# Kernel tuning notes

Hardware: AMD Instinct MI355X
Metric: run time of the kernel (lower is better)

The kernel has to match this reference:

```python
import jax, jax.numpy as jnp
import numpy as np

N, E, F_IN, H, C, G, NCLS, L = 50000, 600000, 128, 4, 64, 64, 3, 3
HC = H * C  # 256


def gatv2_layer(x, src, dst, Wl, bl, Wr, br, att, bias):
    # PyG GATv2Conv (concat=True, negative_slope=0.2, share_weights=False),
    # eval mode so attention dropout is identity.
    n = x.shape[0]
    xl = (x @ Wl + bl).reshape(n, H, C)  # source transform
    xr = (x @ Wr + br).reshape(n, H, C)  # target transform
    e = jax.nn.leaky_relu(xl[src] + xr[dst], negative_slope=0.2)  # [E',H,C]
    score = jnp.einsum('ehc,hc->eh', e, att)                      # [E',H]
    # softmax over incoming edges of each destination node
    mx = jax.ops.segment_max(score, dst, num_segments=n)
    ex = jnp.exp(score - mx[dst])
    denom = jax.ops.segment_sum(ex, dst, num_segments=n)
    alpha = ex / denom[dst]                                       # [E',H]
    out = jax.ops.segment_sum(alpha[..., None] * xl[src], dst, num_segments=n)
    return out.reshape(n, HC) + bias


def setup_inputs() -> dict:
    key = jax.random.key(0)
    ks = jax.random.split(key, 32)
    d = {}
    d['x'] = jax.random.normal(ks[0], (N, F_IN), dtype=jnp.float32)
    d['edge_index'] = jax.random.randint(ks[1], (2, E), 0, N, dtype=jnp.int64)
    d['batch'] = jnp.sort(jax.random.randint(ks[2], (N,), 0, G, dtype=jnp.int64))
    k = 3
    for li in range(L):
        fin = F_IN if li == 0 else HC
        s = 1.0 / np.sqrt(fin)
        d[f'Wl{li}'] = jax.random.normal(ks[k], (fin, HC), dtype=jnp.float32) * s; k += 1
        d[f'bl{li}'] = jnp.zeros((HC,), dtype=jnp.float32)
        d[f'Wr{li}'] = jax.random.normal(ks[k], (fin, HC), dtype=jnp.float32) * s; k += 1
        d[f'br{li}'] = jnp.zeros((HC,), dtype=jnp.float32)
        d[f'att{li}'] = jax.random.normal(ks[k], (H, C), dtype=jnp.float32) * (1.0 / np.sqrt(C)); k += 1
        d[f'bias{li}'] = jnp.zeros((HC,), dtype=jnp.float32)
    d['Wout'] = jax.random.normal(ks[k], (HC, NCLS), dtype=jnp.float32) * (1.0 / np.sqrt(HC))
    d['bout'] = jnp.zeros((NCLS,), dtype=jnp.float32)
    return d


def reference(x, edge_index, batch,
              Wl0, bl0, Wr0, br0, att0, bias0,
              Wl1, bl1, Wr1, br1, att1, bias1,
              Wl2, bl2, Wr2, br2, att2, bias2,
              Wout, bout):
    # add self loops (add_self_loops=True)
    loops = jnp.arange(N, dtype=edge_index.dtype)
    src = jnp.concatenate([edge_index[0], loops])
    dst = jnp.concatenate([edge_index[1], loops])

    h = gatv2_layer(x, src, dst, Wl0, bl0, Wr0, br0, att0, bias0)
    for (Wl, bl, Wr, br, att, bias) in [(Wl1, bl1, Wr1, br1, att1, bias1),
                                        (Wl2, bl2, Wr2, br2, att2, bias2)]:
        h = jax.nn.relu(h)
        h = gatv2_layer(h, src, dst, Wl, bl, Wr, br, att, bias)

    # pooling=0: mean + max over graphs
    counts = jax.ops.segment_sum(jnp.ones((N,), dtype=h.dtype), batch, num_segments=G)
    mean_p = jax.ops.segment_sum(h, batch, num_segments=G) / jnp.maximum(counts, 1.0)[:, None]
    max_p = jax.ops.segment_max(h, batch, num_segments=G)
    p = mean_p + max_p
    # dropout is identity in eval mode
    logits = p @ Wout + bout
    return jax.nn.softmax(logits, axis=1)
```

## Files before the change

### kernel.cpp

```cpp
#include <hip/hip_runtime.h>
#include <math.h>

#define N_NODES 50000
#define N_EDGES 600000
#define F_INPUT 128
#define HCDIM 256
#define NGRAPH 64
#define NCLS 3
#define MPAD 50048
#define SCAN_NB ((N_NODES + 255) / 256)
#define LOG2E 1.4426950408889634f
#define NPART 32
#define COLX_PAD 16
#define TOTAL_E (N_EDGES + N_NODES)
#define PLANE64 ((size_t)N_NODES * 64)
#define EDGE_CHUNKS ((N_NODES + 63) / 64)
#define DBINS 64
#define BSEG (SCAN_NB / 4)
#define GEMM_NB ((MPAD / 128) * 4)

#define HIST_NB   ((N_EDGES + N_NODES + 255) / 256)
#define BND_NB    ((N_NODES + 255) / 256)
#define SPLITX_NB (MPAD * F_INPUT / 4 / 256)
#define ZERO_NB   (((MPAD - N_NODES) * HCDIM / 4 + 255) / 256)
#define WPREP_NB  (512 * (F_INPUT + HCDIM + HCDIM) / 256)
#define HP_NB     (HIST_NB + BND_NB + SPLITX_NB + ZERO_NB + WPREP_NB)
#define FILL_NB   ((TOTAL_E + COLX_PAD + 255) / 256)
#define FG_NB     (FILL_NB + GEMM_NB)

typedef float f32x4 __attribute__((ext_vector_type(4)));
typedef float f32x2 __attribute__((ext_vector_type(2)));
typedef _Float16 f16x8 __attribute__((ext_vector_type(8)));
typedef _Float16 f16x4 __attribute__((ext_vector_type(4)));
typedef _Float16 h2 __attribute__((ext_vector_type(2)));

__device__ __forceinline__ void gl_lds16(const void* g, void* l) {
    __builtin_amdgcn_global_load_lds(
        (const __attribute__((address_space(1))) unsigned int*)g,
        (__attribute__((address_space(3))) unsigned int*)l, 16, 0, 0);
}

__device__ __forceinline__ h2 bch2(unsigned int u) { return __builtin_bit_cast(h2, u); }
__device__ __forceinline__ h2 pk16(float a, float b) {
    return __builtin_bit_cast(h2, __builtin_amdgcn_cvt_pkrtz(a, b));
}

__device__ __forceinline__ int xcd_swizzle(int bid, int nwg) {
    int c = bid & 7, idx = bid >> 3;
    int q = nwg >> 3, r = nwg & 7;
    return (c < r) ? c * (q + 1) + idx : r * (q + 1) + (c - r) * q + idx;
}

__device__ __forceinline__ float quad_reduce_add(float p) {
    int s1 = __builtin_amdgcn_update_dpp(0, __builtin_bit_cast(int, p), 0xB1, 0xF, 0xF, true);
    p += __builtin_bit_cast(float, s1);
    int s2 = __builtin_amdgcn_update_dpp(0, __builtin_bit_cast(int, p), 0x4E, 0xF, 0xF, true);
    p += __builtin_bit_cast(float, s2);
    return p;
}

__device__ __forceinline__ void gemm_body_128(
    const _Float16* __restrict__ A, const _Float16* __restrict__ B, int K,
    const float* __restrict__ bl, const float* __restrict__ br,
    unsigned char* __restrict__ xl8, _Float16* __restrict__ xrh,
    _Float16* sA, _Float16* sB, int bx, int by)
{
    int tid = threadIdx.x;
    int lane = tid & 63, wave = tid >> 6;
    int wm = wave >> 1, wn = wave & 1;
    int row0 = bx * 128;
    int n0 = by * 128;
    int quad = lane >> 4, l16 = lane & 15;

    f32x4 acc[4][4];
    #pragma unroll
    for (int i = 0; i < 4; ++i)
        #pragma unroll
        for (int j = 0; j < 4; ++j)
            acc[i][j] = (f32x4){0.f, 0.f, 0.f, 0.f};

    for (int k0 = 0; k0 < K; k0 += 64) {
        __syncthreads();
        #pragma unroll
        for (int pass = 0; pass < 4; ++pass) {
            int c = tid + pass * 256;
            int r = c >> 3;
            int pl = c & 7;
            int pg = pl ^ (r & 7);
            size_t ga = (size_t)(row0 + r) * K + k0 + pg * 8;
            gl_lds16(A + ga, sA + c * 8);
        }
        #pragma unroll
        for (int pass = 0; pass < 4; ++pass) {
            int c = tid + pass * 256;
            int r = c >> 3;
            int pl = c & 7;
            int pg = pl ^ (r & 7);
            size_t gb = (size_t)(n0 + r) * K + k0 + pg * 8;
            gl_lds16(B + gb, sB + c * 8);
        }
        __syncthreads();

        #pragma unroll
        for (int kk = 0; kk < 2; ++kk) {
            f16x8 fa[4], fb[4];
            #pragma unroll
            for (int i = 0; i < 4; ++i) {
                int rr = wm * 64 + i * 16 + l16;
                int ca = (kk * 4 + quad) ^ (rr & 7);
                fa[i] = *(const f16x8*)&sA[rr * 64 + ca * 8];
            }
            #pragma unroll
            for (int j = 0; j < 4; ++j) {
                int nn = wn * 64 + j * 16 + l16;
                int cb = (kk * 4 + quad) ^ (nn & 7);
                fb[j] = *(const f16x8*)&sB[nn * 64 + cb * 8];
            }
            #pragma unroll
            for (int i = 0; i < 4; ++i)
                #pragma unroll
                for (int j = 0; j < 4; ++j)
                    acc[i][j] = __builtin_amdgcn_mfma_f32_16x16x32_f16(fa[i], fb[j], acc[i][j], 0, 0, 0);
        }
    }

    if (by < 2) {
        int cb0 = by * 128;
        #pragma unroll
        for (int j = 0; j < 4; ++j) {
            int col = cb0 + wn * 64 + j * 16 + l16;
            float bj = bl[col];
            int hh = col >> 6, c64 = col & 63;
            unsigned char* xlp = xl8 + (size_t)hh * PLANE64;
            #pragma unroll
            for (int i = 0; i < 4; ++i) {
                int rbase = row0 + wm * 64 + i * 16 + quad * 4;
                #pragma unroll
                for (int r = 0; r < 4; ++r) {
                    int row = rbase + r;
                    if (row < N_NODES) {
                        float v = acc[i][j][r] + bj;
                        int pk = __builtin_amdgcn_cvt_pk_fp8_f32(v, v, 0, false);
                        xlp[(size_t)row * 64 + c64] = (unsigned char)pk;
                    }
                }
            }
        }
    } else {
        int cb0 = (by - 2) * 128;
        #pragma unroll
        for (int j = 0; j < 4; ++j) {
            int col = cb0 + wn * 64 + j * 16 + l16;
            float bj = br[col];
            int hh = col >> 6, c64 = col & 63;
            _Float16* xrp = xrh + (size_t)hh * PLANE64;
            #pragma unroll
            for (int i = 0; i < 4; ++i) {
                int rbase = row0 + wm * 64 + i * 16 + quad * 4;
                #pragma unroll
                for (int r = 0; r < 4; ++r) {
                    int row = rbase + r;
                    if (row < N_NODES)
                        xrp[(size_t)row * 64 + c64] = (_Float16)(acc[i][j][r] + bj);
                }
            }
        }
    }
}

__global__ void hist_prep_kernel(
    const int* __restrict__ ei, int* __restrict__ deg,
    const int* __restrict__ batch, int* __restrict__ startg, int* __restrict__ endg,
    const float* __restrict__ x, _Float16* __restrict__ A,
    _Float16* __restrict__ Bt0, _Float16* __restrict__ Bt1, _Float16* __restrict__ Bt2,
    const float* __restrict__ Wl0, const float* __restrict__ Wr0,
    const float* __restrict__ Wl1, const float* __restrict__ Wr1,
    const float* __restrict__ Wl2, const float* __restrict__ Wr2)
{
    int b = blockIdx.x;
    if (b < HIST_NB) {
        int i = b * 256 + threadIdx.x;
        if (i >= TOTAL_E) return;
        int d = (i < N_EDGES) ? ei[N_EDGES + i] : (i - N_EDGES);
        atomicAdd(&deg[d], 1);
        return;
    }
    b -= HIST_NB;
    if (b < BND_NB) {
        int i = b * 256 + threadIdx.x;
        if (i >= N_NODES) return;
        int g = batch[i];
        if (i == 0 || batch[i - 1] != g) startg[g] = i;
        if (i == N_NODES - 1 || batch[i + 1] != g) endg[g] = i + 1;
        return;
    }
    b -= BND_NB;
    if (b < SPLITX_NB) {
        int base = (b * 256 + threadIdx.x) * 4;
        int row = base >> 7;
        float4 v = make_float4(0.f, 0.f, 0.f, 0.f);
        if (row < N_NODES) v = *(const float4*)&x[base];
        f16x4 o;
        o.x = (_Float16)v.x; o.y = (_Float16)v.y; o.z = (_Float16)v.z; o.w = (_Float16)v.w;
        *(f16x4*)&A[base] = o;
    } else if (b < SPLITX_NB + ZERO_NB) {
        int i = ((b - SPLITX_NB) * 256 + threadIdx.x) * 4;
        if (i < (MPAD - N_NODES) * HCDIM) {
            f16x4 z = {(_Float16)0.f, (_Float16)0.f, (_Float16)0.f, (_Float16)0.f};
            *(f16x4*)&A[(size_t)N_NODES * HCDIM + i] = z;
        }
    } else {
        int t = (b - SPLITX_NB - ZERO_NB) * 256 + threadIdx.x;
        const float* Wl; const float* Wr; _Float16* Bt; int K;
        if (t < 512 * F_INPUT)            { Wl = Wl0; Wr = Wr0; Bt = Bt0; K = F_INPUT; }
        else if (t < 512 * (F_INPUT + HCDIM)) { t -= 512 * F_INPUT; Wl = Wl1; Wr = Wr1; Bt = Bt1; K = HCDIM; }
        else                              { t -= 512 * (F_INPUT + HCDIM); Wl = Wl2; Wr = Wr2; Bt = Bt2; K = HCDIM; }
        int n = t & 511, k = t >> 9;
        float w = (n < 256) ? Wl[k * 256 + n] : Wr[k * 256 + (n - 256)];
        Bt[n * K + k] = (_Float16)w;
    }
}

__global__ void block_scan_kernel(const int* __restrict__ deg, int* __restrict__ rowptr,
                                  int* __restrict__ bsums) {
    __shared__ int wt[4];
    int b = blockIdx.x, t = threadIdx.x, lane = t & 63, wid = t >> 6;
    int i = b * 256 + t;
    int v = (i < N_NODES) ? deg[i] : 0;
    int x = v;
    #pragma unroll
    for (int off = 1; off < 64; off <<= 1) {
        int y = __shfl_up(x, off, 64);
        if (lane >= off) x += y;
    }
    if (lane == 63) wt[wid] = x;
    __syncthreads();
    if (t == 0) {
        int s = 0;
        #pragma unroll
        for (int j = 0; j < 4; ++j) { int tv = wt[j]; wt[j] = s; s += tv; }
        bsums[b] = s;
    }
    __syncthreads();
    if (i < N_NODES) rowptr[i] = wt[wid] + x - v;
}

__global__ void add_off_kernel(int* __restrict__ rowptr, int* __restrict__ cursor,
                               const int* __restrict__ bsums,
                               const int* __restrict__ deg, int* __restrict__ dhist,
                               int* __restrict__ bcnt) {
    __shared__ int red[256];
    __shared__ int lh[DBINS];
    int b = blockIdx.x, t = threadIdx.x;
    if (t < DBINS) lh[t] = 0;
    red[t] = (t < b) ? bsums[t] : 0;
    __syncthreads();
    for (int off = 128; off > 0; off >>= 1) {
        if (t < off) red[t] += red[t + off];
        __syncthreads();
    }
    int offv = red[0];
    int i = b * 256 + t;
    if (i < N_NODES) {
        int r = rowptr[i] + offv;
        rowptr[i] = r;
        cursor[i] = r;
        int dg = deg[i];
        atomicAdd(&lh[dg < (DBINS - 1) ? dg : (DBINS - 1)], 1);
    }
    if (i == 0) rowptr[N_NODES] = N_EDGES + N_NODES;
    __syncthreads();
    if (t < DBINS) {
        bcnt[b * DBINS + t] = lh[t];
        if (lh[t] != 0) atomicAdd(&dhist[t], lh[t]);
    }
}

__global__ __launch_bounds__(256) void binscan_kernel(const int* __restrict__ dhist,
                                                      int* __restrict__ bcnt) {
    __shared__ int sb[SCAN_NB * DBINS];
    __shared__ int part[4][DBINS];
    __shared__ int binstart[DBINS];
    int t = threadIdx.x;
    for (int i = t; i < SCAN_NB * DBINS; i += 256) sb[i] = bcnt[i];
    if (t < 64) {
        int x = dhist[t];
        #pragma unroll
        for (int off = 1; off < 64; off <<= 1) {
            int y = __shfl_up(x, off, 64);
            if (t >= off) x += y;
        }
        int total = __shfl(x, 63, 64);
        binstart[t] = total - x;
    }
    __syncthreads();
    int l = t & 63, seg = t >> 6;
    int ps = 0;
    for (int b = seg * BSEG; b < (seg + 1) * BSEG; ++b) ps += sb[b * DBINS + l];
    part[seg][l] = ps;
    __syncthreads();
    int off = binstart[l];
    for (int s = 0; s < seg; ++s) off += part[s][l];
    for (int b = seg * BSEG; b < (seg + 1) * BSEG; ++b) {
        int tv = sb[b * DBINS + l];
        sb[b * DBINS + l] = off;
        off += tv;
    }
    __syncthreads();
    for (int i = t; i < SCAN_NB * DBINS; i += 256) bcnt[i] = sb[i];
}

__global__ __launch_bounds__(256) void fill_gemm_kernel(
    const int* __restrict__ ei, int* __restrict__ cursor, int* __restrict__ colx,
    const int* __restrict__ deg, const int* __restrict__ rowptr,
    const int* __restrict__ bcnt, int2* __restrict__ meta,
    const _Float16* __restrict__ A, const _Float16* __restrict__ B,
    const float* __restrict__ bl, const float* __restrict__ br,
    unsigned char* __restrict__ xl8, _Float16* __restrict__ xrh)
{
    __shared__ _Float16 sA[128 * 64], sB[128 * 64];
    int bid = blockIdx.x;
    if (bid < FILL_NB) {
        int* lcnt = (int*)sA;
        int t = threadIdx.x;
        int i = bid * 256 + t;
        if (bid < SCAN_NB) {
            if (t < DBINS) lcnt[t] = 0;
            __syncthreads();
            if (i < N_NODES) {
                int dg = deg[i];
                int bin = dg < (DBINS - 1) ? dg : (DBINS - 1);
                int myr = atomicAdd(&lcnt[bin], 1);
                int pos = bcnt[bid * DBINS + bin] + myr;
                meta[pos] = make_int2(i, rowptr[i] | (dg << 20));
            }
        }
        if (i < TOTAL_E) {
            int s, d;
            if (i < N_EDGES) { s = ei[i]; d = ei[N_EDGES + i]; }
            else             { s = i - N_EDGES; d = s; }
            int pos = atomicAdd(&cursor[d], 1);
            colx[pos] = s * 64;
        } else if (i < TOTAL_E + COLX_PAD) {
            colx[i] = 0;
        }
        return;
    }
    int gbid = bid - FILL_NB;
    int lin = xcd_swizzle(gbid, GEMM_NB);
    gemm_body_128(A, B, F_INPUT, bl, br, xl8, xrh, sA, sB, lin >> 2, lin & 3);
}

__global__ __launch_bounds__(256) void gemm_mfma(
    const _Float16* __restrict__ A, const _Float16* __restrict__ B,
    int K,
    const float* __restrict__ bl, const float* __restrict__ br,
    unsigned char* __restrict__ xl8, _Float16* __restrict__ xrh)
{
    __shared__ _Float16 sA[128 * 64], sB[128 * 64];
    int lin = xcd_swizzle(blockIdx.x, GEMM_NB);
    gemm_body_128(A, B, K, bl, br, xl8, xrh, sA, sB, lin >> 2, lin & 3);
}

__global__ __launch_bounds__(256) void gat_edge(
    const unsigned char* __restrict__ xl8, const _Float16* __restrict__ xrh,
    const float* __restrict__ att, const float* __restrict__ bias,
    const int2* __restrict__ meta, const int* __restrict__ colx,
    _Float16* __restrict__ outh, _Float16* __restrict__ onext, int mode)
{
    int head = blockIdx.x & 3;
    int chunk = blockIdx.x >> 2;
    int wave = threadIdx.x >> 6;
    int lane = threadIdx.x & 63;
    int g  = lane >> 2;
    int ll = lane & 3;
    int slot = chunk * 64 + wave * 16 + g;
    bool valid = slot < N_NODES;
    int saddr = valid ? slot : 0;
    int2 m = meta[saddr];
    int node = m.x;
    int e0 = m.y & 0xFFFFF;
    int cnt = valid ? (int)((unsigned)m.y >> 20) : 0;
    int ch0 = head * 64 + ll * 16;

    int niter = cnt;
    niter = max(niter, __shfl_xor(niter, 4, 64));
    niter = max(niter, __shfl_xor(niter, 8, 64));
    niter = max(niter, __shfl_xor(niter, 16, 64));
    niter = max(niter, __shfl_xor(niter, 32, 64));

    const char* xrrow = (const char*)(xrh + (size_t)head * PLANE64)
                        + ((size_t)node * 64 + ll * 16) * 2;
    uint4 xu0 = *(const uint4*)xrrow;
    uint4 xu1 = *(const uint4*)(xrrow + 16);
    h2 xr[8] = { bch2(xu0.x), bch2(xu0.y), bch2(xu0.z), bch2(xu0.w),
                 bch2(xu1.x), bch2(xu1.y), bch2(xu1.z), bch2(xu1.w) };
    h2 at[8];
    #pragma unroll
    for (int i = 0; i < 8; ++i) {
        float2 av = *(const float2*)&att[ch0 + i * 2];
        at[i] = (h2){(_Float16)(av.x * LOG2E), (_Float16)(av.y * LOG2E)};
    }

    float denom = 0.f;
    f32x2 accp[8];
    #pragma unroll
    for (int i = 0; i < 8; ++i) accp[i] = (f32x2){0.f, 0.f};

    const unsigned char* xb = xl8 + (size_t)head * PLANE64 + ll * 16;
    const h2 slope = {(_Float16)0.2f, (_Float16)0.2f};

    auto process = [&](uint4 dd, int i) {
        unsigned int dw[4] = {dd.x, dd.y, dd.z, dd.w};
        f32x2 lo[4], hi[4];
        h2 hx[8];
        #pragma unroll
        for (int j = 0; j < 4; ++j) {
            lo[j] = __builtin_amdgcn_cvt_pk_f32_fp8(dw[j], false);
            hi[j] = __builtin_amdgcn_cvt_pk_f32_fp8(dw[j], true);
            hx[2 * j]     = pk16(lo[j].x, lo[j].y);
            hx[2 * j + 1] = pk16(hi[j].x, hi[j].y);
        }
        float pa = 0.f, pb = 0.f;
        #pragma unroll
        for (int j = 0; j < 4; ++j) {
            h2 va = hx[j] + xr[j];
            h2 vb = hx[j + 4] + xr[j + 4];
            va = __builtin_elementwise_max(va, va * slope);
            vb = __builtin_elementwise_max(vb, vb * slope);
            pa = __builtin_amdgcn_fdot2(va, at[j], pa, false);
            pb = __builtin_amdgcn_fdot2(vb, at[j + 4], pb, false);
        }
        float p = quad_reduce_add(pa + pb);
        float w = (i < cnt) ? exp2f(p) : 0.f;
        denom += w;
        f32x2 wp = {w, w};
        #pragma unroll
        for (int j = 0; j < 4; ++j) {
            accp[2 * j]     += wp * lo[j];
            accp[2 * j + 1] += wp * hi[j];
        }
    };

    int cx0 = colx[e0];
    int cx1 = colx[e0 + 1];
    int cx2 = colx[e0 + 2];
    int cx3 = colx[e0 + 3];
    uint4 d0 = *(const uint4*)(xb + (unsigned)cx0);
    uint4 d1 = *(const uint4*)(xb + (unsigned)cx1);

    int i = 0;
    for (; i + 2 <= niter; i += 2) {
        uint4 n0 = *(const uint4*)(xb + (unsigned)cx2);
        uint4 n1 = *(const uint4*)(xb + (unsigned)cx3);
        unsigned nx0 = (unsigned)(e0 + i + 4);
        unsigned nx1 = (unsigned)(e0 + i + 5);
        nx0 = nx0 < (unsigned)TOTAL_E ? nx0 : (unsigned)TOTAL_E;
        nx1 = nx1 < (unsigned)TOTAL_E ? nx1 : (unsigned)TOTAL_E;
        cx2 = colx[nx0];
        cx3 = colx[nx1];
        process(d0, i);
        process(d1, i + 1);
        d0 = n0; d1 = n1;
    }
    if (i < niter) process(d0, i);

    if (valid) {
        float inv = 1.f / denom;
        char* orow = (char*)(mode == 0 ? outh : onext)
                     + (size_t)node * (HCDIM * 2) + ch0 * 2;
        h2 o[8];
        #pragma unroll
        for (int i2 = 0; i2 < 8; ++i2) {
            float2 bv = *(const float2*)&bias[ch0 + i2 * 2];
            float v0 = accp[i2].x * inv + bv.x;
            float v1 = accp[i2].y * inv + bv.y;
            if (mode != 0) { v0 = fmaxf(v0, 0.f); v1 = fmaxf(v1, 0.f); }
            o[i2] = pk16(v0, v1);
        }
        uint4 s0 = { __builtin_bit_cast(unsigned int, o[0]), __builtin_bit_cast(unsigned int, o[1]),
                     __builtin_bit_cast(unsigned int, o[2]), __builtin_bit_cast(unsigned int, o[3]) };
        uint4 s1 = { __builtin_bit_cast(unsigned int, o[4]), __builtin_bit_cast(unsigned int, o[5]),
                     __builtin_bit_cast(unsigned int, o[6]), __builtin_bit_cast(unsigned int, o[7]) };
        *(uint4*)orow = s0;
        *(uint4*)(orow + 16) = s1;
    }
}

__global__ __launch_bounds__(256) void pool_partial(
    const _Float16* __restrict__ h, const int* __restrict__ startg,
    const int* __restrict__ endg, float* __restrict__ sumP, float* __restrict__ maxP)
{
    __shared__ float4 sS[4][64];
    __shared__ float4 sM[4][64];
    int g = blockIdx.x >> 5, part = blockIdx.x & (NPART - 1);
    int lane = threadIdx.x & 63;
    int sub = threadIdx.x >> 6;
    int c0 = lane * 4;
    int s = startg[g], e = endg[g];
    float4 sum = make_float4(0.f, 0.f, 0.f, 0.f);
    float4 mx = make_float4(-INFINITY, -INFINITY, -INFINITY, -INFINITY);
    for (int i = s + part * 4 + sub; i < e; i += NPART * 4) {
        uint2 u = *(const uint2*)&h[(size_t)i * HCDIM + c0];
        h2 a = bch2(u.x), b = bch2(u.y);
        float4 v = make_float4((float)a.x, (float)a.y, (float)b.x, (float)b.y);
        sum.x += v.x; sum.y += v.y; sum.z += v.z; sum.w += v.w;
        mx.x = fmaxf(mx.x, v.x); mx.y = fmaxf(mx.y, v.y);
        mx.z = fmaxf(mx.z, v.z); mx.w = fmaxf(mx.w, v.w);
    }
    sS[sub][lane] = sum; sM[sub][lane] = mx;
    __syncthreads();
    if (sub == 0) {
        #pragma unroll
        for (int j = 1; j < 4; ++j) {
            float4 a = sS[j][lane], b = sM[j][lane];
            sum.x += a.x; sum.y += a.y; sum.z += a.z; sum.w += a.w;
            mx.x = fmaxf(mx.x, b.x); mx.y = fmaxf(mx.y, b.y);
            mx.z = fmaxf(mx.z, b.z); mx.w = fmaxf(mx.w, b.w);
        }
        size_t o = (size_t)blockIdx.x * HCDIM + c0;
        *(float4*)&sumP[o] = sum;
        *(float4*)&maxP[o] = mx;
    }
}

__global__ __launch_bounds__(256) void pool_final_logits(
    const float* __restrict__ sumP, const float* __restrict__ maxP,
    const int* __restrict__ startg, const int* __restrict__ endg,
    const float* __restrict__ Wout, const float* __restrict__ bout,
    float* __restrict__ out)
{
    __shared__ float red[256];
    __shared__ float lg[NCLS];
    int g = blockIdx.x, c = threadIdx.x;
    float s = 0.f, m = -INFINITY;
    #pragma unroll 8
    for (int part = 0; part < NPART; ++part) {
        size_t o = (size_t)(g * NPART + part) * HCDIM + c;
        s += sumP[o];
        m = fmaxf(m, maxP[o]);
    }
    int cnt = endg[g] - startg[g];
    float inv = 1.f / fmaxf((float)cnt, 1.f);
    float pv = s * inv + m;

    for (int j = 0; j < NCLS; ++j) {
        red[c] = pv * Wout[c * NCLS + j];
        __syncthreads();
        for (int off = 128; off > 0; off >>= 1) {
            if (c < off) red[c] += red[c + off];
            __syncthreads();
        }
        if (c == 0) lg[j] = red[0] + bout[j];
        __syncthreads();
    }
    if (c == 0) {
        float mx = fmaxf(lg[0], fmaxf(lg[1], lg[2]));
        float e0 = __expf(lg[0] - mx), e1 = __expf(lg[1] - mx), e2 = __expf(lg[2] - mx);
        float invs = 1.f / (e0 + e1 + e2);
        out[g * NCLS + 0] = e0 * invs;
        out[g * NCLS + 1] = e1 * invs;
        out[g * NCLS + 2] = e2 * invs;
    }
}

extern "C" void kernel_launch(void* const* d_in, const int* in_sizes, int n_in,
                              void* d_out, int out_size, void* d_ws, size_t ws_size,
                              hipStream_t stream) {
    const float* x     = (const float*)d_in[0];
    const int*   ei    = (const int*)d_in[1];
    const int*   batch = (const int*)d_in[2];
    const float *Wl[3], *bl[3], *Wr[3], *br[3], *att[3], *bias[3];
    for (int li = 0; li < 3; ++li) {
        int b = 3 + li * 6;
        Wl[li]   = (const float*)d_in[b + 0];
        bl[li]   = (const float*)d_in[b + 1];
        Wr[li]   = (const float*)d_in[b + 2];
        br[li]   = (const float*)d_in[b + 3];
        att[li]  = (const float*)d_in[b + 4];
        bias[li] = (const float*)d_in[b + 5];
    }
    const float* Wout = (const float*)d_in[21];
    const float* bout = (const float*)d_in[22];
    float* out = (float*)d_out;

    size_t off = 0;
    char* wsb = (char*)d_ws;
    auto alloc = [&](size_t bytes) -> char* {
        char* ptr = wsb + off;
        off += (bytes + 255) & ~(size_t)255;
        return ptr;
    };
    int* zblk    = (int*)alloc((N_NODES + 2 * NGRAPH + DBINS) * sizeof(int));
    int* deg     = zblk;
    int* startg  = zblk + N_NODES;
    int* endg    = zblk + N_NODES + NGRAPH;
    int* dhist   = zblk + N_NODES + 2 * NGRAPH;
    int* rowptr  = (int*)alloc((N_NODES + 1) * sizeof(int));
    int* cursor  = (int*)alloc(N_NODES * sizeof(int));
    int* bsums   = (int*)alloc(256 * sizeof(int));
    int* bcnt    = (int*)alloc(SCAN_NB * DBINS * sizeof(int));
    int2* meta   = (int2*)alloc(N_NODES * sizeof(int2));
    int* colx    = (int*)alloc((size_t)(N_EDGES + N_NODES + COLX_PAD) * sizeof(int));
    _Float16* Abuf = (_Float16*)alloc((size_t)MPAD * HCDIM * sizeof(_Float16));
    _Float16* Bt[3];
    for (int li = 0; li < 3; ++li) {
        int K = (li == 0) ? F_INPUT : HCDIM;
        Bt[li] = (_Float16*)alloc((size_t)512 * K * sizeof(_Float16));
    }
    unsigned char* xl8 = (unsigned char*)alloc((size_t)N_NODES * HCDIM);
    _Float16* xrh  = (_Float16*)alloc((size_t)N_NODES * HCDIM * sizeof(_Float16));
    _Float16* hbuf = (_Float16*)alloc((size_t)N_NODES * HCDIM * sizeof(_Float16));
    float* sumP    = (float*)alloc((size_t)NGRAPH * NPART * HCDIM * sizeof(float));
    float* maxP    = (float*)alloc((size_t)NGRAPH * NPART * HCDIM * sizeof(float));

    hipMemsetAsync(zblk, 0, (N_NODES + 2 * NGRAPH + DBINS) * sizeof(int), stream);

    hist_prep_kernel<<<HP_NB, 256, 0, stream>>>(
        ei, deg, batch, startg, endg,
        x, Abuf, Bt[0], Bt[1], Bt[2],
        Wl[0], Wr[0], Wl[1], Wr[1], Wl[2], Wr[2]);
    block_scan_kernel<<<SCAN_NB, 256, 0, stream>>>(deg, rowptr, bsums);
    add_off_kernel<<<SCAN_NB, 256, 0, stream>>>(rowptr, cursor, bsums, deg, dhist, bcnt);
    binscan_kernel<<<1, 256, 0, stream>>>(dhist, bcnt);

    fill_gemm_kernel<<<FG_NB, 256, 0, stream>>>(
        ei, cursor, colx, deg, rowptr, bcnt, meta,
        Abuf, Bt[0], bl[0], br[0], xl8, xrh);
    gat_edge<<<EDGE_CHUNKS * 4, 256, 0, stream>>>(
        xl8, xrh, att[0], bias[0], meta, colx, nullptr, Abuf, 1);

    for (int li = 1; li < 3; ++li) {
        gemm_mfma<<<GEMM_NB, 256, 0, stream>>>(
            Abuf, Bt[li], HCDIM, bl[li], br[li], xl8, xrh);
        if (li < 2) {
            gat_edge<<<EDGE_CHUNKS * 4, 256, 0, stream>>>(
                xl8, xrh, att[li], bias[li], meta, colx, nullptr, Abuf, 1);
        } else {
            gat_edge<<<EDGE_CHUNKS * 4, 256, 0, stream>>>(
                xl8, xrh, att[li], bias[li], meta, colx, hbuf, nullptr, 0);
        }
    }

    pool_partial<<<NGRAPH * NPART, 256, 0, stream>>>(hbuf, startg, endg, sumP, maxP);
    pool_final_logits<<<NGRAPH, 256, 0, stream>>>(sumP, maxP, startg, endg, Wout, bout, out);
}
```

Baseline: 455.4 us.

## Halve GEMM row tile to 64, simplify XCD mapping, deepen edge gather prefetch

Shrinks the projection GEMM tile from 128 to 64 rows, which doubles the block count and cuts LDS and accumulator registers, aiming for better occupancy and load balance. It swaps the general XCD swizzle for a simpler contiguous mapping that assumes the block count divides by 8. The edge aggregation loop now keeps four gathered feature rows in flight instead of two, to hide gather latency better. The cost is more register pressure in the edge kernel and less B-tile reuse per block in the GEMM. Reading colx[e0+4] and colx[e0+5] before the loop has no clamp, which is safe only as long as the COLX_PAD padding covers it.

```diff
diff --git a/kernel.cpp b/kernel.cpp
--- a/kernel.cpp
+++ b/kernel.cpp
@@ -17,7 +17,8 @@
 #define EDGE_CHUNKS ((N_NODES + 63) / 64)
 #define DBINS 64
 #define BSEG (SCAN_NB / 4)
-#define GEMM_NB ((MPAD / 128) * 4)
+#define GEMM_NB ((MPAD / 64) * 4)
+#define GEMM_QPX (GEMM_NB / 8)
 
 #define HIST_NB   ((N_EDGES + N_NODES + 255) / 256)
 #define BND_NB    ((N_NODES + 255) / 256)
@@ -45,12 +46,6 @@
     return __builtin_bit_cast(h2, __builtin_amdgcn_cvt_pkrtz(a, b));
 }
 
-__device__ __forceinline__ int xcd_swizzle(int bid, int nwg) {
-    int c = bid & 7, idx = bid >> 3;
-    int q = nwg >> 3, r = nwg & 7;
-    return (c < r) ? c * (q + 1) + idx : r * (q + 1) + (c - r) * q + idx;
-}
-
 __device__ __forceinline__ float quad_reduce_add(float p) {
     int s1 = __builtin_amdgcn_update_dpp(0, __builtin_bit_cast(int, p), 0xB1, 0xF, 0xF, true);
     p += __builtin_bit_cast(float, s1);
@@ -59,7 +54,7 @@
     return p;
 }
 
-__device__ __forceinline__ void gemm_body_128(
+__device__ __forceinline__ void gemm_body_64(
     const _Float16* __restrict__ A, const _Float16* __restrict__ B, int K,
     const float* __restrict__ bl, const float* __restrict__ br,
     unsigned char* __restrict__ xl8, _Float16* __restrict__ xrh,
@@ -68,13 +63,13 @@
     int tid = threadIdx.x;
     int lane = tid & 63, wave = tid >> 6;
     int wm = wave >> 1, wn = wave & 1;
-    int row0 = bx * 128;
+    int row0 = bx * 64;
     int n0 = by * 128;
     int quad = lane >> 4, l16 = lane & 15;
 
-    f32x4 acc[4][4];
+    f32x4 acc[2][4];
     #pragma unroll
-    for (int i = 0; i < 4; ++i)
+    for (int i = 0; i < 2; ++i)
         #pragma unroll
         for (int j = 0; j < 4; ++j)
             acc[i][j] = (f32x4){0.f, 0.f, 0.f, 0.f};
@@ -82,7 +77,7 @@
     for (int k0 = 0; k0 < K; k0 += 64) {
         __syncthreads();
         #pragma unroll
-        for (int pass = 0; pass < 4; ++pass) {
+        for (int pass = 0; pass < 2; ++pass) {
             int c = tid + pass * 256;
             int r = c >> 3;
             int pl = c & 7;
@@ -103,10 +98,10 @@
 
         #pragma unroll
         for (int kk = 0; kk < 2; ++kk) {
-            f16x8 fa[4], fb[4];
+            f16x8 fa[2], fb[4];
             #pragma unroll
-            for (int i = 0; i < 4; ++i) {
-                int rr = wm * 64 + i * 16 + l16;
+            for (int i = 0; i < 2; ++i) {
+                int rr = wm * 32 + i * 16 + l16;
                 int ca = (kk * 4 + quad) ^ (rr & 7);
                 fa[i] = *(const f16x8*)&sA[rr * 64 + ca * 8];
             }
@@ -117,7 +112,7 @@
                 fb[j] = *(const f16x8*)&sB[nn * 64 + cb * 8];
             }
             #pragma unroll
-            for (int i = 0; i < 4; ++i)
+            for (int i = 0; i < 2; ++i)
                 #pragma unroll
                 for (int j = 0; j < 4; ++j)
                     acc[i][j] = __builtin_amdgcn_mfma_f32_16x16x32_f16(fa[i], fb[j], acc[i][j], 0, 0, 0);
@@ -133,8 +128,8 @@
             int hh = col >> 6, c64 = col & 63;
             unsigned char* xlp = xl8 + (size_t)hh * PLANE64;
             #pragma unroll
-            for (int i = 0; i < 4; ++i) {
-                int rbase = row0 + wm * 64 + i * 16 + quad * 4;
+            for (int i = 0; i < 2; ++i) {
+                int rbase = row0 + wm * 32 + i * 16 + quad * 4;
                 #pragma unroll
                 for (int r = 0; r < 4; ++r) {
                     int row = rbase + r;
@@ -155,8 +150,8 @@
             int hh = col >> 6, c64 = col & 63;
             _Float16* xrp = xrh + (size_t)hh * PLANE64;
             #pragma unroll
-            for (int i = 0; i < 4; ++i) {
-                int rbase = row0 + wm * 64 + i * 16 + quad * 4;
+            for (int i = 0; i < 2; ++i) {
+                int rbase = row0 + wm * 32 + i * 16 + quad * 4;
                 #pragma unroll
                 for (int r = 0; r < 4; ++r) {
                     int row = rbase + r;
@@ -318,7 +313,7 @@
     const float* __restrict__ bl, const float* __restrict__ br,
     unsigned char* __restrict__ xl8, _Float16* __restrict__ xrh)
 {
-    __shared__ _Float16 sA[128 * 64], sB[128 * 64];
+    __shared__ _Float16 sA[64 * 64], sB[128 * 64];
     int bid = blockIdx.x;
     if (bid < FILL_NB) {
         int* lcnt = (int*)sA;
@@ -347,8 +342,8 @@
         return;
     }
     int gbid = bid - FILL_NB;
-    int lin = xcd_swizzle(gbid, GEMM_NB);
-    gemm_body_128(A, B, F_INPUT, bl, br, xl8, xrh, sA, sB, lin >> 2, lin & 3);
+    int lin = (gbid & 7) * GEMM_QPX + (gbid >> 3);
+    gemm_body_64(A, B, F_INPUT, bl, br, xl8, xrh, sA, sB, lin >> 2, lin & 3);
 }
 
 __global__ __launch_bounds__(256) void gemm_mfma(
@@ -357,9 +352,10 @@
     const float* __restrict__ bl, const float* __restrict__ br,
     unsigned char* __restrict__ xl8, _Float16* __restrict__ xrh)
 {
-    __shared__ _Float16 sA[128 * 64], sB[128 * 64];
-    int lin = xcd_swizzle(blockIdx.x, GEMM_NB);
-    gemm_body_128(A, B, K, bl, br, xl8, xrh, sA, sB, lin >> 2, lin & 3);
+    __shared__ _Float16 sA[64 * 64], sB[128 * 64];
+    int bid = blockIdx.x;
+    int lin = (bid & 7) * GEMM_QPX + (bid >> 3);
+    gemm_body_64(A, B, K, bl, br, xl8, xrh, sA, sB, lin >> 2, lin & 3);
 }
 
 __global__ __launch_bounds__(256) void gat_edge(
@@ -442,26 +438,27 @@
         }
     };
 
-    int cx0 = colx[e0];
-    int cx1 = colx[e0 + 1];
-    int cx2 = colx[e0 + 2];
-    int cx3 = colx[e0 + 3];
-    uint4 d0 = *(const uint4*)(xb + (unsigned)cx0);
-    uint4 d1 = *(const uint4*)(xb + (unsigned)cx1);
+    uint4 d0 = *(const uint4*)(xb + (unsigned)colx[e0]);
+    uint4 d1 = *(const uint4*)(xb + (unsigned)colx[e0 + 1]);
+    uint4 d2 = *(const uint4*)(xb + (unsigned)colx[e0 + 2]);
+    uint4 d3 = *(const uint4*)(xb + (unsigned)colx[e0 + 3]);
+    int cx_a = colx[e0 + 4];
+    int cx_b = colx[e0 + 5];
 
     int i = 0;
     for (; i + 2 <= niter; i += 2) {
-        uint4 n0 = *(const uint4*)(xb + (unsigned)cx2);
-        uint4 n1 = *(const uint4*)(xb + (unsigned)cx3);
-        unsigned nx0 = (unsigned)(e0 + i + 4);
-        unsigned nx1 = (unsigned)(e0 + i + 5);
+        uint4 n0 = *(const uint4*)(xb + (unsigned)cx_a);
+        uint4 n1 = *(const uint4*)(xb + (unsigned)cx_b);
+        unsigned nx0 = (unsigned)(e0 + i + 6);
+        unsigned nx1 = (unsigned)(e0 + i + 7);
         nx0 = nx0 < (unsigned)TOTAL_E ? nx0 : (unsigned)TOTAL_E;
         nx1 = nx1 < (unsigned)TOTAL_E ? nx1 : (unsigned)TOTAL_E;
-        cx2 = colx[nx0];
-        cx3 = colx[nx1];
+        cx_a = colx[nx0];
+        cx_b = colx[nx1];
         process(d0, i);
         process(d1, i + 1);
-        d0 = n0; d1 = n1;
+        d0 = d2; d1 = d3;
+        d2 = n0; d3 = n1;
     }
     if (i < niter) process(d0, i);
 
```

Measured after the change: 406.0 us. 10.9% less time.
